# Kernel tuning notes

Measured on AMD Instinct MI355X. Metric: run time of the kernel, lower is better.

## Reference

```python
import jax, jax.numpy as jnp
import numpy as np


def setup_inputs() -> dict:
    key = jax.random.key(0)
    k1, k2, k3 = jax.random.split(key, 3)
    B, H, S, D = 2, 8, 4096, 64
    queries = jax.random.normal(k1, (B, H, S, D), dtype=jnp.float32)
    keys = jax.random.normal(k2, (B, H, S, D), dtype=jnp.float32)
    values = jax.random.normal(k3, (B, H, S, D), dtype=jnp.float32)
    mask = jnp.zeros((1, 1, S, S), dtype=jnp.float32)
    return {"queries": queries, "keys": keys, "values": values, "d_k": D, "mask": mask}


def reference(queries, keys, values, d_k, mask):
    # scores: [B, H, Sq, Sk]
    scale = 1.0 / jnp.sqrt(jnp.asarray(d_k, dtype=queries.dtype))
    scores = jnp.einsum("bhqd,bhkd->bhqk", queries, keys) * scale
    scores = scores + (-1e9) * mask  # additive mask, broadcasts over B, H
    weights = jax.nn.softmax(scores, axis=-1)
    return jnp.einsum("bhqk,bhkd->bhqd", weights, values)
```

## Files before the change

kernel.cpp:

```cpp
#include <hip/hip_runtime.h>

#define S_LEN 4096
#define DHEAD 64
#define BK    64
#define NT    (S_LEN / BK)
#define NBH   16
#define KPAD  72
#define BQ    128
#define TILE_HALFS (BK * DHEAD)
#define WS_KV_HALFS ((size_t)NBH * NT * TILE_HALFS)

typedef __fp16   pk16x2 __attribute__((ext_vector_type(2)));
typedef _Float16 half4v __attribute__((ext_vector_type(4)));
typedef _Float16 half8  __attribute__((ext_vector_type(8)));
typedef float    f32x4  __attribute__((ext_vector_type(4)));
typedef float    f32x16 __attribute__((ext_vector_type(16)));
typedef unsigned uint2v __attribute__((ext_vector_type(2)));

#define MFMA32(a, b, c) __builtin_amdgcn_mfma_f32_32x32x16_f16(a, b, c, 0, 0, 0)

__device__ __forceinline__ void gl_lds16(const _Float16* g, _Float16* l) {
    __builtin_amdgcn_global_load_lds(
        (const __attribute__((address_space(1))) unsigned int*)g,
        (__attribute__((address_space(3))) unsigned int*)l, 16, 0, 0);
}

__device__ __forceinline__ unsigned pk2u(float a, float b) {
    union { pk16x2 p; unsigned u; } x;
    x.p = __builtin_amdgcn_cvt_pkrtz(a, b);
    return x.u;
}

__device__ __forceinline__ uint2v pls(unsigned x, unsigned y) {
    return __builtin_amdgcn_permlane32_swap(x, y, false, false);
}
__device__ __forceinline__ float xmax32(float v) {
    uint2v r = pls(__float_as_uint(v), __float_as_uint(v));
    return fmaxf(__uint_as_float(r.x), __uint_as_float(r.y));
}
__device__ __forceinline__ float xadd32(float v) {
    uint2v r = pls(__float_as_uint(v), __float_as_uint(v));
    return __uint_as_float(r.x) + __uint_as_float(r.y);
}

__global__ void mask_flag_kernel(const float4* __restrict__ mask, int* __restrict__ flag) {
    const long stride = 2048L * 256;
    long i = (long)blockIdx.x * 256 + threadIdx.x;
    int nz = 0;
    #pragma unroll
    for (int it = 0; it < 8; ++it) {
        float4 a = mask[i + it * stride];
        nz |= (a.x != 0.f) | (a.y != 0.f) | (a.z != 0.f) | (a.w != 0.f);
    }
    if (__any(nz)) {
        if ((threadIdx.x & 63) == 0) atomicOr(flag, 1);
    }
}

__global__ void conv_kernel(const float* __restrict__ Kg, const float* __restrict__ Vg,
                            const float* __restrict__ mask,
                            _Float16* __restrict__ wsK, _Float16* __restrict__ wsV,
                            int* __restrict__ flag) {
    const int tid  = threadIdx.x;
    const int tile = blockIdx.x;
    __shared__ __align__(16) _Float16 T[64][64];

    if (blockIdx.y == 0) {
        const float* Ksrc = Kg + (long)tile * TILE_HALFS;
        _Float16*    dst  = wsK + (long)tile * TILE_HALFS;
        #pragma unroll
        for (int it = 0; it < 2; ++it) {
            int m = tid + it * 256;
            int r = m >> 3, c = m & 7;
            const float4* s4 = (const float4*)(Ksrc + r * DHEAD + ((c ^ (r & 7)) << 3));
            float4 a = s4[0], b = s4[1];
            union { pk16x2 p[4]; half8 h; } u;
            u.p[0] = __builtin_amdgcn_cvt_pkrtz(a.x, a.y);
            u.p[1] = __builtin_amdgcn_cvt_pkrtz(a.z, a.w);
            u.p[2] = __builtin_amdgcn_cvt_pkrtz(b.x, b.y);
            u.p[3] = __builtin_amdgcn_cvt_pkrtz(b.z, b.w);
            *(half8*)(dst + m * 8) = u.h;
        }
    } else if (blockIdx.y == 1) {
        const float* Vsrc = Vg + (long)tile * TILE_HALFS;
        const int r  = tid >> 2;
        const int d0 = (tid & 3) << 4;
        const float4* s4 = (const float4*)(Vsrc + r * DHEAD + d0);
        float vv[16];
        *(float4*)&vv[0]  = s4[0];
        *(float4*)&vv[4]  = s4[1];
        *(float4*)&vv[8]  = s4[2];
        *(float4*)&vv[12] = s4[3];
        #pragma unroll
        for (int j = 0; j < 16; j += 2) {
            pk16x2 p = __builtin_amdgcn_cvt_pkrtz(vv[j], vv[j + 1]);
            T[d0 + j][r]     = *((_Float16*)&p);
            T[d0 + j + 1][r] = *((_Float16*)&p + 1);
        }
        __syncthreads();
        _Float16* dst = wsV + (long)tile * TILE_HALFS;
        #pragma unroll
        for (int it = 0; it < 2; ++it) {
            int m = tid + it * 256;
            int d = m >> 3, c = m & 7;
            *(half8*)(dst + m * 8) = *(const half8*)&T[d][(c ^ (d & 7)) << 3];
        }
    } else {
        const float4* m4 = (const float4*)mask;
        const long stride = 1024L * 256;
        long i = (long)blockIdx.x * 256 + tid;
        int nz = 0;
        #pragma unroll
        for (int it = 0; it < 16; ++it) {
            float4 a = m4[i + it * stride];
            nz |= (a.x != 0.f) | (a.y != 0.f) | (a.z != 0.f) | (a.w != 0.f);
        }
        if (__any(nz)) {
            if ((tid & 63) == 0) atomicOr(flag, 1);
        }
    }
}

template <int SPLIT>
__global__ __launch_bounds__(256, 4) void attn32_kernel(
    const float* __restrict__ Q, const _Float16* __restrict__ KW,
    const _Float16* __restrict__ VW, const int* __restrict__ dkp,
    const float* __restrict__ mask, const int* __restrict__ maskflag,
    float* __restrict__ O1, float* __restrict__ O2, float* __restrict__ ML)
{
    const int fid = blockIdx.x;
    int bh, half, qt;
    if (SPLIT == 2) {
        const int L = (fid & 7) * 128 + (fid >> 3);
        bh = L >> 6; half = (L >> 5) & 1; qt = L & 31;
    } else {
        const int L = (fid & 7) * 64 + (fid >> 3);
        bh = L >> 5; half = 0; qt = L & 31;
    }
    const int HT  = NT / SPLIT;
    const int kt0 = half * HT;

    const int tid  = threadIdx.x;
    const int wave = tid >> 6;
    const int lane = tid & 63;
    const int l31  = lane & 31;
    const int h    = lane >> 5;
    const int cx   = lane & 7;
    const bool hib = (lane >= 32);

    const long base = (long)bh * S_LEN * DHEAD;
    const float* Qh = Q + base;
    const _Float16* gk = KW + (long)bh * (NT * TILE_HALFS);
    const _Float16* gv = VW + (long)bh * (NT * TILE_HALFS);

    const int q0 = qt * 128 + wave * 32;
    const float csq  = rsqrtf((float)dkp[0]) * 1.44269504088896f;
    const float mfac = -1e9f * 1.44269504088896f;
    const bool use_mask = (maskflag[0] != 0);

    __shared__ __align__(16) _Float16 KT[2][TILE_HALFS];
    __shared__ __align__(16) _Float16 VT[2][TILE_HALFS];

    half8 qf[4];
    #pragma unroll
    for (int ks = 0; ks < 4; ++ks) {
        const float4* src = (const float4*)(Qh + (long)(q0 + l31) * DHEAD + ks * 16 + h * 8);
        float4 a = src[0], b = src[1];
        union { unsigned u[4]; half8 h8; } u;
        u.u[0] = pk2u(a.x * csq, a.y * csq);
        u.u[1] = pk2u(a.z * csq, a.w * csq);
        u.u[2] = pk2u(b.x * csq, b.y * csq);
        u.u[3] = pk2u(b.z * csq, b.w * csq);
        qf[ks] = u.h8;
    }

    auto stage = [&](int kt, int bb) {
        const _Float16* k8 = gk + (long)kt * TILE_HALFS + tid * 8;
        const _Float16* v8 = gv + (long)kt * TILE_HALFS + tid * 8;
        gl_lds16(k8,        &KT[bb][tid * 8]);
        gl_lds16(k8 + 2048, &KT[bb][2048 + tid * 8]);
        gl_lds16(v8,        &VT[bb][tid * 8]);
        gl_lds16(v8 + 2048, &VT[bb][2048 + tid * 8]);
    };

    f32x16 o0 = {0.f,0.f,0.f,0.f,0.f,0.f,0.f,0.f,0.f,0.f,0.f,0.f,0.f,0.f,0.f,0.f};
    f32x16 o1 = o0;
    float m_i = -INFINITY;
    float l_i = 0.0f;

    stage(kt0, 0);
    __syncthreads();

    for (int lt = 0; lt < HT; ++lt) {
        const int kt = kt0 + lt;
        const int b  = lt & 1;
        if (lt + 1 < HT) stage(kt + 1, b ^ 1);

        f32x16 s0 = {0.f,0.f,0.f,0.f,0.f,0.f,0.f,0.f,0.f,0.f,0.f,0.f,0.f,0.f,0.f,0.f};
        f32x16 s1 = s0;
        __builtin_amdgcn_s_setprio(1);
        #pragma unroll
        for (int ks = 0; ks < 4; ++ks) {
            const int off = (((2 * ks + h) ^ cx) << 3);
            half8 a0 = *(const half8*)&KT[b][(l31 << 6) + off];
            half8 a1 = *(const half8*)&KT[b][2048 + (l31 << 6) + off];
            s0 = MFMA32(a0, qf[ks], s0);
            s1 = MFMA32(a1, qf[ks], s1);
        }
        __builtin_amdgcn_s_setprio(0);

        if (use_mask) {
            const float* mrow = mask + (long)(q0 + l31) * S_LEN + kt * BK;
            #pragma unroll
            for (int r = 0; r < 16; ++r) {
                const int k = (r & 3) + ((r >> 2) << 3) + (h << 2);
                s0[r] += mfac * mrow[k];
                s1[r] += mfac * mrow[32 + k];
            }
        }

        {
            float t[8];
            #pragma unroll
            for (int i = 0; i < 8; ++i)
                t[i] = fmaxf(fmaxf(s0[2*i], s0[2*i+1]), fmaxf(s1[2*i], s1[2*i+1]));
            float mx = fmaxf(fmaxf(fmaxf(t[0], t[1]), fmaxf(t[2], t[3])),
                             fmaxf(fmaxf(t[4], t[5]), fmaxf(t[6], t[7])));
            mx = xmax32(mx);
            const bool need = __any(mx > m_i);
            const float mnew = need ? fmaxf(m_i, mx) : m_i;
            float ra = 0.f, rb = 0.f;
            #pragma unroll
            for (int r = 0; r < 16; ++r) {
                float p0 = __builtin_amdgcn_exp2f(s0[r] - mnew);
                float p1 = __builtin_amdgcn_exp2f(s1[r] - mnew);
                s0[r] = p0; s1[r] = p1;
                ra += p0; rb += p1;
            }
            float rsum = xadd32(ra + rb);
            if (need) {
                const float alpha = __builtin_amdgcn_exp2f(m_i - mnew);
                #pragma unroll
                for (int r = 0; r < 16; ++r) {
                    const int qr = (r & 3) + ((r >> 2) << 3) + (h << 2);
                    float a_r = __shfl(alpha, qr, 64);
                    o0[r] *= a_r; o1[r] *= a_r;
                }
                l_i = alpha * l_i + rsum;
                m_i = mnew;
            } else {
                l_i += rsum;
            }
        }

        unsigned plo[16], phi[16];
        #pragma unroll
        for (int d = 0; d < 8; ++d) {
            uint2v r0 = pls(pk2u(s0[2*d], s0[2*d+1]), pk2u(s0[2*d], s0[2*d+1]));
            plo[d] = r0.x; phi[d] = r0.y;
            uint2v r1 = pls(pk2u(s1[2*d], s1[2*d+1]), pk2u(s1[2*d], s1[2*d+1]));
            plo[8 + d] = r1.x; phi[8 + d] = r1.y;
        }

        __builtin_amdgcn_s_setprio(1);
        #pragma unroll
        for (int s = 0; s < 4; ++s) {
            const int kb = s >> 1, tq = s & 1, bs = kb * 8 + 4 * tq;
            union { unsigned u[4]; half8 h8; } pa;
            pa.u[0] = hib ? plo[bs + 2] : plo[bs + 0];
            pa.u[1] = hib ? plo[bs + 3] : plo[bs + 1];
            pa.u[2] = hib ? phi[bs + 2] : phi[bs + 0];
            pa.u[3] = hib ? phi[bs + 3] : phi[bs + 1];
            const int off = (((2 * s + h) ^ cx) << 3);
            half8 v0 = *(const half8*)&VT[b][(l31 << 6) + off];
            half8 v1 = *(const half8*)&VT[b][2048 + (l31 << 6) + off];
            o0 = MFMA32(pa.h8, v0, o0);
            o1 = MFMA32(pa.h8, v1, o1);
        }
        __builtin_amdgcn_s_setprio(0);

        if (lt + 1 < HT) __syncthreads();
    }

    if (SPLIT == 2) {
        float* dst = ((half == 0) ? O1 : O2) + base;
        #pragma unroll
        for (int r = 0; r < 16; ++r) {
            const int qr = (r & 3) + ((r >> 2) << 3) + (h << 2);
            const long row = (long)(q0 + qr) * DHEAD;
            dst[row + l31]      = o0[r];
            dst[row + 32 + l31] = o1[r];
        }
        if (!hib) {
            float2* ml = (float2*)ML + (long)(half * NBH + bh) * S_LEN + q0 + l31;
            *ml = make_float2(m_i, l_i);
        }
    } else {
        float* dst = O1 + base;
        #pragma unroll
        for (int r = 0; r < 16; ++r) {
            const int qr = (r & 3) + ((r >> 2) << 3) + (h << 2);
            float lq = __shfl(l_i, qr, 64);
            float inv = __builtin_amdgcn_rcpf(lq);
            const long row = (long)(q0 + qr) * DHEAD;
            dst[row + l31]      = o0[r] * inv;
            dst[row + 32 + l31] = o1[r] * inv;
        }
    }
}

__global__ __launch_bounds__(256) void combine_kernel(
    float* __restrict__ O1, const float* __restrict__ O2,
    const float* __restrict__ ML)
{
    const long flat = (long)blockIdx.x * 256 + threadIdx.x;
    const int  dg = (int)(flat & 15);
    const long q  = (flat >> 4) & (S_LEN - 1);
    const int  bh = (int)(flat >> 16);
    const float2 ml1 = ((const float2*)ML)[(long)(0 * NBH + bh) * S_LEN + q];
    const float2 ml2 = ((const float2*)ML)[(long)(1 * NBH + bh) * S_LEN + q];
    const float m  = fmaxf(ml1.x, ml2.x);
    const float a1 = __builtin_amdgcn_exp2f(ml1.x - m);
    const float a2 = __builtin_amdgcn_exp2f(ml2.x - m);
    const float inv = __builtin_amdgcn_rcpf(ml1.y * a1 + ml2.y * a2);
    const long idx = ((long)bh * S_LEN + q) * DHEAD + dg * 4;
    float4 x1 = *(const float4*)&O1[idx];
    float4 x2 = *(const float4*)&O2[idx];
    float4 r;
    r.x = (x1.x * a1 + x2.x * a2) * inv;
    r.y = (x1.y * a1 + x2.y * a2) * inv;
    r.z = (x1.z * a1 + x2.z * a2) * inv;
    r.w = (x1.w * a1 + x2.w * a2) * inv;
    *(float4*)&O1[idx] = r;
}

__global__ __launch_bounds__(256, 2) void attn_kernel_fb(
    const float* __restrict__ Q, const float* __restrict__ K,
    const float* __restrict__ V, const int* __restrict__ dk,
    const float* __restrict__ mask, const int* __restrict__ maskflag,
    float* __restrict__ O)
{
    const int qt   = blockIdx.x;
    const int bh   = blockIdx.y;
    const int tid  = threadIdx.x;
    const int wave = tid >> 6;
    const int lane = tid & 63;
    const int l15  = lane & 15;
    const int quad = lane >> 4;

    const long base = (long)bh * S_LEN * DHEAD;
    const float* Qh = Q + base;
    const float* Kh = K + base;
    const float* Vh = V + base;
    float*       Oh = O + base;

    const int q0 = qt * BQ + wave * 32;
    const float csq  = rsqrtf((float)dk[0]) * 1.44269504088896f;
    const float mfac = -1e9f * 1.44269504088896f;
    const bool use_mask = (maskflag[0] != 0);

    __shared__ __align__(16) _Float16 Kt[2][BK][KPAD];
    __shared__ __align__(16) _Float16 Vt[2][DHEAD * KPAD];
    __shared__ __align__(16) _Float16 Pw[4][32][KPAD];

    half8 qf[2][2];
    #pragma unroll
    for (int f = 0; f < 2; ++f) {
        #pragma unroll
        for (int kc = 0; kc < 2; ++kc) {
            const float4* src = (const float4*)(Qh + (long)(q0 + f*16 + l15) * DHEAD + kc*32 + quad*8);
            float4 a = src[0], b = src[1];
            union { pk16x2 p[4]; half8 h; } u;
            u.p[0] = __builtin_amdgcn_cvt_pkrtz(a.x*csq, a.y*csq);
            u.p[1] = __builtin_amdgcn_cvt_pkrtz(a.z*csq, a.w*csq);
            u.p[2] = __builtin_amdgcn_cvt_pkrtz(b.x*csq, b.y*csq);
            u.p[3] = __builtin_amdgcn_cvt_pkrtz(b.z*csq, b.w*csq);
            qf[f][kc] = u.h;
        }
    }

    const int kr  = tid >> 2;
    const int ks  = tid & 3;
    const int vrp = tid >> 3;
    const int vdq = tid & 7;
    const float* Kb = Kh + (long)kr * DHEAD + ks * 16;
    const float* Vb = Vh + (long)(2 * vrp) * DHEAD + vdq * 8;
    const int vcol = (((vrp >> 2) ^ vdq) << 3) + ((2 * vrp) & 7);
    const int vd0  = vdq * 8;

    float4 kf[4], vf[4];
    auto load_tile = [&](int kt) {
        const float4* kp  = (const float4*)(Kb + (long)kt * BK * DHEAD);
        kf[0] = kp[0]; kf[1] = kp[1]; kf[2] = kp[2]; kf[3] = kp[3];
        const float4* vp0 = (const float4*)(Vb + (long)kt * BK * DHEAD);
        const float4* vp1 = (const float4*)(Vb + (long)kt * BK * DHEAD + DHEAD);
        vf[0] = vp0[0]; vf[1] = vp0[1]; vf[2] = vp1[0]; vf[3] = vp1[1];
    };
    auto store_tile = [&](int b) {
        union { pk16x2 p[4]; half8 h; } u0, u1;
        u0.p[0] = __builtin_amdgcn_cvt_pkrtz(kf[0].x, kf[0].y);
        u0.p[1] = __builtin_amdgcn_cvt_pkrtz(kf[0].z, kf[0].w);
        u0.p[2] = __builtin_amdgcn_cvt_pkrtz(kf[1].x, kf[1].y);
        u0.p[3] = __builtin_amdgcn_cvt_pkrtz(kf[1].z, kf[1].w);
        u1.p[0] = __builtin_amdgcn_cvt_pkrtz(kf[2].x, kf[2].y);
        u1.p[1] = __builtin_amdgcn_cvt_pkrtz(kf[2].z, kf[2].w);
        u1.p[2] = __builtin_amdgcn_cvt_pkrtz(kf[3].x, kf[3].y);
        u1.p[3] = __builtin_amdgcn_cvt_pkrtz(kf[3].z, kf[3].w);
        *(half8*)&Kt[b][kr][ks*16]     = u0.h;
        *(half8*)&Kt[b][kr][ks*16 + 8] = u1.h;
        _Float16* vt = &Vt[b][0];
        *(pk16x2*)&vt[(vd0+0)*KPAD + vcol] = __builtin_amdgcn_cvt_pkrtz(vf[0].x, vf[2].x);
        *(pk16x2*)&vt[(vd0+1)*KPAD + vcol] = __builtin_amdgcn_cvt_pkrtz(vf[0].y, vf[2].y);
        *(pk16x2*)&vt[(vd0+2)*KPAD + vcol] = __builtin_amdgcn_cvt_pkrtz(vf[0].z, vf[2].z);
        *(pk16x2*)&vt[(vd0+3)*KPAD + vcol] = __builtin_amdgcn_cvt_pkrtz(vf[0].w, vf[2].w);
        *(pk16x2*)&vt[(vd0+4)*KPAD + vcol] = __builtin_amdgcn_cvt_pkrtz(vf[1].x, vf[3].x);
        *(pk16x2*)&vt[(vd0+5)*KPAD + vcol] = __builtin_amdgcn_cvt_pkrtz(vf[1].y, vf[3].y);
        *(pk16x2*)&vt[(vd0+6)*KPAD + vcol] = __builtin_amdgcn_cvt_pkrtz(vf[1].z, vf[3].z);
        *(pk16x2*)&vt[(vd0+7)*KPAD + vcol] = __builtin_amdgcn_cvt_pkrtz(vf[1].w, vf[3].w);
    };

    f32x4 o[2][4];
    #pragma unroll
    for (int f = 0; f < 2; ++f)
        #pragma unroll
        for (int dt = 0; dt < 4; ++dt) o[f][dt] = (f32x4){0.f, 0.f, 0.f, 0.f};
    float m_i[2] = {-INFINITY, -INFINITY};
    float l_i[2] = {0.0f, 0.0f};

    load_tile(0);
    store_tile(0);
    __syncthreads();

    for (int kt = 0; kt < NT; ++kt) {
        const int b = kt & 1;
        if (kt + 1 < NT) load_tile(kt + 1);

        f32x4 st[2][4];
        #pragma unroll
        for (int f = 0; f < 2; ++f)
            #pragma unroll
            for (int nt = 0; nt < 4; ++nt) st[f][nt] = (f32x4){0.f,0.f,0.f,0.f};
        #pragma unroll
        for (int nt = 0; nt < 4; ++nt) {
            #pragma unroll
            for (int kc = 0; kc < 2; ++kc) {
                half8 af = *(const half8*)&Kt[b][nt*16 + l15][kc*32 + quad*8];
                st[0][nt] = __builtin_amdgcn_mfma_f32_16x16x32_f16(af, qf[0][kc], st[0][nt], 0, 0, 0);
                st[1][nt] = __builtin_amdgcn_mfma_f32_16x16x32_f16(af, qf[1][kc], st[1][nt], 0, 0, 0);
            }
        }

        if (use_mask) {
            #pragma unroll
            for (int f = 0; f < 2; ++f) {
                const long mrow = (long)(q0 + f*16 + l15) * S_LEN + kt*BK;
                #pragma unroll
                for (int nt = 0; nt < 4; ++nt)
                    #pragma unroll
                    for (int r = 0; r < 4; ++r)
                        st[f][nt][r] += mfac * mask[mrow + nt*16 + quad*4 + r];
            }
        }

        float alpha[2];
        #pragma unroll
        for (int f = 0; f < 2; ++f) {
            float mx = fmaxf(fmaxf(fmaxf(st[f][0][0], st[f][0][1]), fmaxf(st[f][0][2], st[f][0][3])),
                             fmaxf(fmaxf(st[f][1][0], st[f][1][1]), fmaxf(st[f][1][2], st[f][1][3])));
            float mx2 = fmaxf(fmaxf(fmaxf(st[f][2][0], st[f][2][1]), fmaxf(st[f][2][2], st[f][2][3])),
                              fmaxf(fmaxf(st[f][3][0], st[f][3][1]), fmaxf(st[f][3][2], st[f][3][3])));
            mx = fmaxf(mx, mx2);
            mx = fmaxf(mx, __shfl_xor(mx, 16, 64));
            mx = fmaxf(mx, __shfl_xor(mx, 32, 64));
            float mnew = fmaxf(m_i[f], mx);
            float rsum = 0.0f;
            #pragma unroll
            for (int nt = 0; nt < 4; ++nt) {
                #pragma unroll
                for (int r = 0; r < 4; ++r) {
                    float p = __builtin_amdgcn_exp2f(st[f][nt][r] - mnew);
                    st[f][nt][r] = p;
                    rsum += p;
                }
            }
            rsum += __shfl_xor(rsum, 16, 64);
            rsum += __shfl_xor(rsum, 32, 64);
            alpha[f] = __builtin_amdgcn_exp2f(m_i[f] - mnew);
            l_i[f] = alpha[f] * l_i[f] + rsum;
            m_i[f] = mnew;
        }

        #pragma unroll
        for (int f = 0; f < 2; ++f)
            #pragma unroll
            for (int r = 0; r < 4; ++r) {
                float a_r = __shfl(alpha[f], quad*4 + r, 64);
                #pragma unroll
                for (int dt = 0; dt < 4; ++dt) o[f][dt][r] *= a_r;
            }

        #pragma unroll
        for (int f = 0; f < 2; ++f)
            #pragma unroll
            for (int nt = 0; nt < 4; ++nt) {
                union { pk16x2 p[2]; half4v h; } up;
                up.p[0] = __builtin_amdgcn_cvt_pkrtz(st[f][nt][0], st[f][nt][1]);
                up.p[1] = __builtin_amdgcn_cvt_pkrtz(st[f][nt][2], st[f][nt][3]);
                *(half4v*)&Pw[wave][f*16 + l15][nt*16 + quad*4] = up.h;
            }

        #pragma unroll
        for (int kc2 = 0; kc2 < 2; ++kc2) {
            half8 pa0 = *(const half8*)&Pw[wave][l15][kc2*32 + quad*8];
            half8 pa1 = *(const half8*)&Pw[wave][16 + l15][kc2*32 + quad*8];
            #pragma unroll
            for (int dt = 0; dt < 4; ++dt) {
                const int row = dt*16 + l15;
                const int pb  = (4*kc2 + quad) ^ (row >> 3);
                half8 vb = *(const half8*)&Vt[b][row*KPAD + pb*8];
                o[0][dt] = __builtin_amdgcn_mfma_f32_16x16x32_f16(pa0, vb, o[0][dt], 0, 0, 0);
                o[1][dt] = __builtin_amdgcn_mfma_f32_16x16x32_f16(pa1, vb, o[1][dt], 0, 0, 0);
            }
        }

        if (kt + 1 < NT) {
            store_tile((kt + 1) & 1);
            __syncthreads();
        }
    }

    #pragma unroll
    for (int f = 0; f < 2; ++f) {
        #pragma unroll
        for (int r = 0; r < 4; ++r) {
            float lq = __shfl(l_i[f], quad*4 + r, 64);
            float linv = __builtin_amdgcn_rcpf(lq);
            const long row = (long)(q0 + f*16 + quad*4 + r) * DHEAD;
            #pragma unroll
            for (int dt = 0; dt < 4; ++dt)
                Oh[row + dt*16 + l15] = o[f][dt][r] * linv;
        }
    }
}

extern "C" void kernel_launch(void* const* d_in, const int* in_sizes, int n_in,
                              void* d_out, int out_size, void* d_ws, size_t ws_size,
                              hipStream_t stream) {
    const float* Q    = (const float*)d_in[0];
    const float* K    = (const float*)d_in[1];
    const float* V    = (const float*)d_in[2];
    const int*   dk   = (const int*)d_in[3];
    const float* mask = (const float*)d_in[4];
    float* out = (float*)d_out;
    int* flag = (int*)d_ws;

    (void)hipMemsetAsync(flag, 0, sizeof(int), stream);

    const size_t KV_BYTES = 2 * WS_KV_HALFS * sizeof(_Float16);
    const size_t O2_BYTES = (size_t)NBH * S_LEN * DHEAD * sizeof(float);
    const size_t ML_BYTES = 2ull * NBH * S_LEN * 2 * sizeof(float);
    const size_t NEED_BASE  = 256 + KV_BYTES;
    const size_t NEED_SPLIT = NEED_BASE + O2_BYTES + ML_BYTES;

    if (ws_size >= NEED_BASE) {
        _Float16* wsK = (_Float16*)((char*)d_ws + 256);
        _Float16* wsV = wsK + WS_KV_HALFS;
        conv_kernel<<<dim3(NBH * NT, 3), 256, 0, stream>>>(K, V, mask, wsK, wsV, flag);
        if (ws_size >= NEED_SPLIT) {
            float* O2 = (float*)((char*)d_ws + 256 + KV_BYTES);
            float* ML = (float*)((char*)d_ws + 256 + KV_BYTES + O2_BYTES);
            attn32_kernel<2><<<1024, 256, 0, stream>>>(Q, wsK, wsV, dk, mask, flag, out, O2, ML);
            combine_kernel<<<4096, 256, 0, stream>>>(out, O2, ML);
        } else {
            attn32_kernel<1><<<512, 256, 0, stream>>>(Q, wsK, wsV, dk, mask, flag, out, nullptr, nullptr);
        }
    } else {
        mask_flag_kernel<<<2048, 256, 0, stream>>>((const float4*)mask, flag);
        dim3 grid(S_LEN / BQ, NBH);
        attn_kernel_fb<<<grid, 256, 0, stream>>>(Q, K, V, dk, mask, flag, out);
    }
}
```

Measured before the change: 270.6 us.

## Fuse split-KV combine into attention kernel via last-block atomic counter

The separate combine kernel is removed. Each block pair that shares a query tile now bumps an atomic counter, and whichever block finishes second merges the two partial outputs in place. The row-sum l is now accumulated with an extra MFMA against a ones vector instead of a VALU reduction. Rescaling is skipped unless the running max grows by more than 8, a lazy-rescale threshold. The P permutation is also simplified. These changes aim to cut a kernel launch and a full extra pass over O, plus VALU work, at the cost of one more MFMA per step and a tail where only some blocks do the combine.

```diff
diff --git a/kernel.cpp b/kernel.cpp
--- a/kernel.cpp
+++ b/kernel.cpp
@@ -121,24 +121,19 @@
     }
 }
 
-template <int SPLIT>
-__global__ __launch_bounds__(256, 4) void attn32_kernel(
+__global__ __launch_bounds__(256, 4) void attn32c_kernel(
     const float* __restrict__ Q, const _Float16* __restrict__ KW,
     const _Float16* __restrict__ VW, const int* __restrict__ dkp,
-    const float* __restrict__ mask, const int* __restrict__ maskflag,
+    const float* __restrict__ mask, int* __restrict__ ctrl,
     float* __restrict__ O1, float* __restrict__ O2, float* __restrict__ ML)
 {
-    const int fid = blockIdx.x;
-    int bh, half, qt;
-    if (SPLIT == 2) {
-        const int L = (fid & 7) * 128 + (fid >> 3);
-        bh = L >> 6; half = (L >> 5) & 1; qt = L & 31;
-    } else {
-        const int L = (fid & 7) * 64 + (fid >> 3);
-        bh = L >> 5; half = 0; qt = L & 31;
-    }
-    const int HT  = NT / SPLIT;
-    const int kt0 = half * HT;
+    const int bid = blockIdx.x;
+    const int L   = (bid & 7) * 128 + (bid >> 3);
+    const int bh  = L >> 6;
+    const int hf  = (L >> 5) & 1;
+    const int qt  = L & 31;
+    const int HT  = NT / 2;
+    const int kt0 = hf * HT;
 
     const int tid  = threadIdx.x;
     const int wave = tid >> 6;
@@ -146,20 +141,20 @@
     const int l31  = lane & 31;
     const int h    = lane >> 5;
     const int cx   = lane & 7;
-    const bool hib = (lane >= 32);
-
-    const long base = (long)bh * S_LEN * DHEAD;
-    const float* Qh = Q + base;
+
+    const long gbase = (long)bh * S_LEN * DHEAD;
+    const float* Qh = Q + gbase;
     const _Float16* gk = KW + (long)bh * (NT * TILE_HALFS);
     const _Float16* gv = VW + (long)bh * (NT * TILE_HALFS);
 
     const int q0 = qt * 128 + wave * 32;
     const float csq  = rsqrtf((float)dkp[0]) * 1.44269504088896f;
     const float mfac = -1e9f * 1.44269504088896f;
-    const bool use_mask = (maskflag[0] != 0);
+    const bool use_mask = (ctrl[0] != 0);
 
     __shared__ __align__(16) _Float16 KT[2][TILE_HALFS];
     __shared__ __align__(16) _Float16 VT[2][TILE_HALFS];
+    __shared__ int s_last;
 
     half8 qf[4];
     #pragma unroll
@@ -174,6 +169,10 @@
         qf[ks] = u.h8;
     }
 
+    half8 vones;
+    #pragma unroll
+    for (int j = 0; j < 8; ++j) vones[j] = (_Float16)1.0f;
+
     auto stage = [&](int kt, int bb) {
         const _Float16* k8 = gk + (long)kt * TILE_HALFS + tid * 8;
         const _Float16* v8 = gv + (long)kt * TILE_HALFS + tid * 8;
@@ -185,8 +184,8 @@
 
     f32x16 o0 = {0.f,0.f,0.f,0.f,0.f,0.f,0.f,0.f,0.f,0.f,0.f,0.f,0.f,0.f,0.f,0.f};
     f32x16 o1 = o0;
+    f32x16 ol = o0;
     float m_i = -INFINITY;
-    float l_i = 0.0f;
 
     stage(kt0, 0);
     __syncthreads();
@@ -211,6 +210,204 @@
 
         if (use_mask) {
             const float* mrow = mask + (long)(q0 + l31) * S_LEN + kt * BK;
+            #pragma unroll
+            for (int r = 0; r < 16; ++r) {
+                const int k = (r & 3) + ((r >> 2) << 3) + (h << 2);
+                s0[r] += mfac * mrow[k];
+                s1[r] += mfac * mrow[32 + k];
+            }
+        }
+
+        {
+            float t[8];
+            #pragma unroll
+            for (int i = 0; i < 8; ++i)
+                t[i] = fmaxf(fmaxf(s0[2*i], s0[2*i+1]), fmaxf(s1[2*i], s1[2*i+1]));
+            float mx = fmaxf(fmaxf(fmaxf(t[0], t[1]), fmaxf(t[2], t[3])),
+                             fmaxf(fmaxf(t[4], t[5]), fmaxf(t[6], t[7])));
+            mx = xmax32(mx);
+            const bool need = __any(mx > m_i + 8.0f);
+            const float mnew = need ? fmaxf(m_i, mx) : m_i;
+            #pragma unroll
+            for (int r = 0; r < 16; ++r) {
+                s0[r] = __builtin_amdgcn_exp2f(s0[r] - mnew);
+                s1[r] = __builtin_amdgcn_exp2f(s1[r] - mnew);
+            }
+            if (need) {
+                const float alpha = __builtin_amdgcn_exp2f(m_i - mnew);
+                #pragma unroll
+                for (int r = 0; r < 16; ++r) {
+                    const int qr = (r & 3) + ((r >> 2) << 3) + (h << 2);
+                    float a_r = __shfl(alpha, qr, 64);
+                    o0[r] *= a_r; o1[r] *= a_r; ol[r] *= a_r;
+                }
+                m_i = mnew;
+            }
+        }
+
+        unsigned w[16];
+        #pragma unroll
+        for (int d = 0; d < 8; ++d) {
+            w[d]     = pk2u(s0[2*d], s0[2*d+1]);
+            w[8 + d] = pk2u(s1[2*d], s1[2*d+1]);
+        }
+
+        __builtin_amdgcn_s_setprio(1);
+        #pragma unroll
+        for (int si = 0; si < 4; ++si) {
+            const int bs = (si >> 1) * 8 + (si & 1) * 4;
+            uint2v r0 = pls(w[bs + 0], w[bs + 2]);
+            uint2v r1 = pls(w[bs + 1], w[bs + 3]);
+            union { unsigned u[4]; half8 h8; } pa;
+            pa.u[0] = r0.x; pa.u[1] = r1.x; pa.u[2] = r0.y; pa.u[3] = r1.y;
+            const int off = (((2 * si + h) ^ cx) << 3);
+            half8 v0 = *(const half8*)&VT[b][(l31 << 6) + off];
+            half8 v1 = *(const half8*)&VT[b][2048 + (l31 << 6) + off];
+            o0 = MFMA32(pa.h8, v0, o0);
+            o1 = MFMA32(pa.h8, v1, o1);
+            ol = MFMA32(pa.h8, vones, ol);
+        }
+        __builtin_amdgcn_s_setprio(0);
+
+        if (lt + 1 < HT) __syncthreads();
+    }
+
+    float* dst = ((hf == 0) ? O1 : O2) + gbase;
+    #pragma unroll
+    for (int r = 0; r < 16; ++r) {
+        const int qr = (r & 3) + ((r >> 2) << 3) + (h << 2);
+        const long row = (long)(q0 + qr) * DHEAD;
+        dst[row + l31]      = o0[r];
+        dst[row + 32 + l31] = o1[r];
+    }
+    {
+        const int rr = l31 & 15;
+        float lv = ol[0];
+        #pragma unroll
+        for (int r = 1; r < 16; ++r) lv = (rr == r) ? ol[r] : lv;
+        const int qre = (rr & 3) + ((rr >> 2) << 3) + (h << 2);
+        const float mv = __shfl(m_i, qre, 64);
+        if (l31 < 16) {
+            float2* ml = (float2*)ML + (long)(hf * NBH + bh) * S_LEN + q0 + qre;
+            *ml = make_float2(mv, lv);
+        }
+    }
+
+    __syncthreads();
+    if (tid == 0) {
+        __threadfence();
+        int old = atomicAdd(ctrl + 64 + (bh * 32 + qt), 1);
+        if (old == 1) __threadfence();
+        s_last = old;
+    }
+    __syncthreads();
+
+    if (s_last == 1) {
+        const int q  = qt * 128 + (tid >> 1);
+        const int dc = (tid & 1) * 32;
+        const float2 ml1 = ((const float2*)ML)[(long)(0 * NBH + bh) * S_LEN + q];
+        const float2 ml2 = ((const float2*)ML)[(long)(NBH + bh) * S_LEN + q];
+        const float m   = fmaxf(ml1.x, ml2.x);
+        const float a1  = __builtin_amdgcn_exp2f(ml1.x - m);
+        const float a2  = __builtin_amdgcn_exp2f(ml2.x - m);
+        const float inv = __builtin_amdgcn_rcpf(ml1.y * a1 + ml2.y * a2);
+        float*       p1 = O1 + gbase + (long)q * DHEAD + dc;
+        const float* p2 = O2 + gbase + (long)q * DHEAD + dc;
+        #pragma unroll
+        for (int j = 0; j < 8; ++j) {
+            float4 x1 = *(const float4*)&p1[j * 4];
+            float4 x2 = *(const float4*)&p2[j * 4];
+            float4 r4;
+            r4.x = (x1.x * a1 + x2.x * a2) * inv;
+            r4.y = (x1.y * a1 + x2.y * a2) * inv;
+            r4.z = (x1.z * a1 + x2.z * a2) * inv;
+            r4.w = (x1.w * a1 + x2.w * a2) * inv;
+            *(float4*)&p1[j * 4] = r4;
+        }
+    }
+}
+
+__global__ __launch_bounds__(256, 4) void attn32_s1_kernel(
+    const float* __restrict__ Q, const _Float16* __restrict__ KW,
+    const _Float16* __restrict__ VW, const int* __restrict__ dkp,
+    const float* __restrict__ mask, const int* __restrict__ maskflag,
+    float* __restrict__ O1)
+{
+    const int fid = blockIdx.x;
+    const int L = (fid & 7) * 64 + (fid >> 3);
+    const int bh = L >> 5;
+    const int qt = L & 31;
+
+    const int tid  = threadIdx.x;
+    const int wave = tid >> 6;
+    const int lane = tid & 63;
+    const int l31  = lane & 31;
+    const int h    = lane >> 5;
+    const int cx   = lane & 7;
+    const bool hib = (lane >= 32);
+
+    const long base = (long)bh * S_LEN * DHEAD;
+    const float* Qh = Q + base;
+    const _Float16* gk = KW + (long)bh * (NT * TILE_HALFS);
+    const _Float16* gv = VW + (long)bh * (NT * TILE_HALFS);
+
+    const int q0 = qt * 128 + wave * 32;
+    const float csq  = rsqrtf((float)dkp[0]) * 1.44269504088896f;
+    const float mfac = -1e9f * 1.44269504088896f;
+    const bool use_mask = (maskflag[0] != 0);
+
+    __shared__ __align__(16) _Float16 KT[2][TILE_HALFS];
+    __shared__ __align__(16) _Float16 VT[2][TILE_HALFS];
+
+    half8 qf[4];
+    #pragma unroll
+    for (int ks = 0; ks < 4; ++ks) {
+        const float4* src = (const float4*)(Qh + (long)(q0 + l31) * DHEAD + ks * 16 + h * 8);
+        float4 a = src[0], b = src[1];
+        union { unsigned u[4]; half8 h8; } u;
+        u.u[0] = pk2u(a.x * csq, a.y * csq);
+        u.u[1] = pk2u(a.z * csq, a.w * csq);
+        u.u[2] = pk2u(b.x * csq, b.y * csq);
+        u.u[3] = pk2u(b.z * csq, b.w * csq);
+        qf[ks] = u.h8;
+    }
+
+    auto stage = [&](int kt, int bb) {
+        const _Float16* k8 = gk + (long)kt * TILE_HALFS + tid * 8;
+        const _Float16* v8 = gv + (long)kt * TILE_HALFS + tid * 8;
+        gl_lds16(k8,        &KT[bb][tid * 8]);
+        gl_lds16(k8 + 2048, &KT[bb][2048 + tid * 8]);
+        gl_lds16(v8,        &VT[bb][tid * 8]);
+        gl_lds16(v8 + 2048, &VT[bb][2048 + tid * 8]);
+    };
+
+    f32x16 o0 = {0.f,0.f,0.f,0.f,0.f,0.f,0.f,0.f,0.f,0.f,0.f,0.f,0.f,0.f,0.f,0.f};
+    f32x16 o1 = o0;
+    float m_i = -INFINITY;
+    float l_i = 0.0f;
+
+    stage(0, 0);
+    __syncthreads();
+
+    for (int lt = 0; lt < NT; ++lt) {
+        const int b = lt & 1;
+        if (lt + 1 < NT) stage(lt + 1, b ^ 1);
+
+        f32x16 s0 = {0.f,0.f,0.f,0.f,0.f,0.f,0.f,0.f,0.f,0.f,0.f,0.f,0.f,0.f,0.f,0.f};
+        f32x16 s1 = s0;
+        __builtin_amdgcn_s_setprio(1);
+        #pragma unroll
+        for (int ks = 0; ks < 4; ++ks) {
+            const int off = (((2 * ks + h) ^ cx) << 3);
+            half8 a0 = *(const half8*)&KT[b][(l31 << 6) + off];
+            half8 a1 = *(const half8*)&KT[b][2048 + (l31 << 6) + off];
+            s0 = MFMA32(a0, qf[ks], s0);
+            s1 = MFMA32(a1, qf[ks], s1);
+        }
+        __builtin_amdgcn_s_setprio(0);
+
+        if (use_mask) {
+            const float* mrow = mask + (long)(q0 + l31) * S_LEN + lt * BK;
             #pragma unroll
             for (int r = 0; r < 16; ++r) {
                 const int k = (r & 3) + ((r >> 2) << 3) + (h << 2);
@@ -265,7 +462,7 @@
         __builtin_amdgcn_s_setprio(1);
         #pragma unroll
         for (int s = 0; s < 4; ++s) {
-            const int kb = s >> 1, tq = s & 1, bs = kb * 8 + 4 * tq;
+            const int bs = (s >> 1) * 8 + (s & 1) * 4;
             union { unsigned u[4]; half8 h8; } pa;
             pa.u[0] = hib ? plo[bs + 2] : plo[bs + 0];
             pa.u[1] = hib ? plo[bs + 3] : plo[bs + 1];
@@ -279,59 +476,19 @@
         }
         __builtin_amdgcn_s_setprio(0);
 
-        if (lt + 1 < HT) __syncthreads();
-    }
-
-    if (SPLIT == 2) {
-        float* dst = ((half == 0) ? O1 : O2) + base;
-        #pragma unroll
-        for (int r = 0; r < 16; ++r) {
-            const int qr = (r & 3) + ((r >> 2) << 3) + (h << 2);
-            const long row = (long)(q0 + qr) * DHEAD;
-            dst[row + l31]      = o0[r];
-            dst[row + 32 + l31] = o1[r];
-        }
-        if (!hib) {
-            float2* ml = (float2*)ML + (long)(half * NBH + bh) * S_LEN + q0 + l31;
-            *ml = make_float2(m_i, l_i);
-        }
-    } else {
-        float* dst = O1 + base;
-        #pragma unroll
-        for (int r = 0; r < 16; ++r) {
-            const int qr = (r & 3) + ((r >> 2) << 3) + (h << 2);
-            float lq = __shfl(l_i, qr, 64);
-            float inv = __builtin_amdgcn_rcpf(lq);
-            const long row = (long)(q0 + qr) * DHEAD;
-            dst[row + l31]      = o0[r] * inv;
-            dst[row + 32 + l31] = o1[r] * inv;
-        }
-    }
-}
-
-__global__ __launch_bounds__(256) void combine_kernel(
-    float* __restrict__ O1, const float* __restrict__ O2,
-    const float* __restrict__ ML)
-{
-    const long flat = (long)blockIdx.x * 256 + threadIdx.x;
-    const int  dg = (int)(flat & 15);
-    const long q  = (flat >> 4) & (S_LEN - 1);
-    const int  bh = (int)(flat >> 16);
-    const float2 ml1 = ((const float2*)ML)[(long)(0 * NBH + bh) * S_LEN + q];
-    const float2 ml2 = ((const float2*)ML)[(long)(1 * NBH + bh) * S_LEN + q];
-    const float m  = fmaxf(ml1.x, ml2.x);
-    const float a1 = __builtin_amdgcn_exp2f(ml1.x - m);
-    const float a2 = __builtin_amdgcn_exp2f(ml2.x - m);
-    const float inv = __builtin_amdgcn_rcpf(ml1.y * a1 + ml2.y * a2);
-    const long idx = ((long)bh * S_LEN + q) * DHEAD + dg * 4;
-    float4 x1 = *(const float4*)&O1[idx];
-    float4 x2 = *(const float4*)&O2[idx];
-    float4 r;
-    r.x = (x1.x * a1 + x2.x * a2) * inv;
-    r.y = (x1.y * a1 + x2.y * a2) * inv;
-    r.z = (x1.z * a1 + x2.z * a2) * inv;
-    r.w = (x1.w * a1 + x2.w * a2) * inv;
-    *(float4*)&O1[idx] = r;
+        if (lt + 1 < NT) __syncthreads();
+    }
+
+    float* dst = O1 + base;
+    #pragma unroll
+    for (int r = 0; r < 16; ++r) {
+        const int qr = (r & 3) + ((r >> 2) << 3) + (h << 2);
+        float lq = __shfl(l_i, qr, 64);
+        float inv = __builtin_amdgcn_rcpf(lq);
+        const long row = (long)(q0 + qr) * DHEAD;
+        dst[row + l31]      = o0[r] * inv;
+        dst[row + 32 + l31] = o1[r] * inv;
+    }
 }
 
 __global__ __launch_bounds__(256, 2) void attn_kernel_fb(
@@ -552,31 +709,31 @@
     const int*   dk   = (const int*)d_in[3];
     const float* mask = (const float*)d_in[4];
     float* out = (float*)d_out;
-    int* flag = (int*)d_ws;
-
-    (void)hipMemsetAsync(flag, 0, sizeof(int), stream);
-
+    int* ctrl = (int*)d_ws;
+
+    (void)hipMemsetAsync(ctrl, 0, 4096, stream);
+
+    const size_t CTRL     = 4096;
     const size_t KV_BYTES = 2 * WS_KV_HALFS * sizeof(_Float16);
     const size_t O2_BYTES = (size_t)NBH * S_LEN * DHEAD * sizeof(float);
     const size_t ML_BYTES = 2ull * NBH * S_LEN * 2 * sizeof(float);
-    const size_t NEED_BASE  = 256 + KV_BYTES;
-    const size_t NEED_SPLIT = NEED_BASE + O2_BYTES + ML_BYTES;
+    const size_t NEED_BASE = CTRL + KV_BYTES;
+    const size_t NEED_FULL = NEED_BASE + O2_BYTES + ML_BYTES;
 
     if (ws_size >= NEED_BASE) {
-        _Float16* wsK = (_Float16*)((char*)d_ws + 256);
+        _Float16* wsK = (_Float16*)((char*)d_ws + CTRL);
         _Float16* wsV = wsK + WS_KV_HALFS;
-        conv_kernel<<<dim3(NBH * NT, 3), 256, 0, stream>>>(K, V, mask, wsK, wsV, flag);
-        if (ws_size >= NEED_SPLIT) {
-            float* O2 = (float*)((char*)d_ws + 256 + KV_BYTES);
-            float* ML = (float*)((char*)d_ws + 256 + KV_BYTES + O2_BYTES);
-            attn32_kernel<2><<<1024, 256, 0, stream>>>(Q, wsK, wsV, dk, mask, flag, out, O2, ML);
-            combine_kernel<<<4096, 256, 0, stream>>>(out, O2, ML);
+        conv_kernel<<<dim3(NBH * NT, 3), 256, 0, stream>>>(K, V, mask, wsK, wsV, ctrl);
+        if (ws_size >= NEED_FULL) {
+            float* O2 = (float*)((char*)d_ws + CTRL + KV_BYTES);
+            float* ML = (float*)((char*)d_ws + CTRL + KV_BYTES + O2_BYTES);
+            attn32c_kernel<<<1024, 256, 0, stream>>>(Q, wsK, wsV, dk, mask, ctrl, out, O2, ML);
         } else {
-            attn32_kernel<1><<<512, 256, 0, stream>>>(Q, wsK, wsV, dk, mask, flag, out, nullptr, nullptr);
+            attn32_s1_kernel<<<512, 256, 0, stream>>>(Q, wsK, wsV, dk, mask, ctrl, out);
         }
     } else {
-        mask_flag_kernel<<<2048, 256, 0, stream>>>((const float4*)mask, flag);
+        mask_flag_kernel<<<2048, 256, 0, stream>>>((const float4*)mask, ctrl);
         dim3 grid(S_LEN / BQ, NBH);
-        attn_kernel_fb<<<grid, 256, 0, stream>>>(Q, K, V, dk, mask, flag, out);
-    }
-}
+        attn_kernel_fb<<<grid, 256, 0, stream>>>(Q, K, V, dk, mask, ctrl, out);
+    }
+}
```

Result: slower. 323.7 us (+19.6%).

## Fuse split-KV halves into one 512-thread block with in-LDS combine

Applied to the files above, without the earlier changes.

Replaces the two-pass split-KV attention (1024 blocks of 256 threads plus a separate combine kernel through global O2/ML buffers) with one 512-thread block per query tile. Each 256-thread half processes half the key tiles and the two partial results are merged through shared memory at the end. The change also computes the row sums with an extra MFMA against a ones vector instead of shuffle reductions, and skips the max rescale unless the new max exceeds the old one by more than 8 in the exp2 domain. It removes the extra kernel launch and the global round-trip of partial outputs. In exchange it doubles LDS per block, which may reduce occupancy, and the lazy rescale relies on fp16 probabilities staying in range.

```diff
diff --git a/kernel.cpp b/kernel.cpp
--- a/kernel.cpp
+++ b/kernel.cpp
@@ -37,10 +37,6 @@
 __device__ __forceinline__ float xmax32(float v) {
     uint2v r = pls(__float_as_uint(v), __float_as_uint(v));
     return fmaxf(__uint_as_float(r.x), __uint_as_float(r.y));
-}
-__device__ __forceinline__ float xadd32(float v) {
-    uint2v r = pls(__float_as_uint(v), __float_as_uint(v));
-    return __uint_as_float(r.x) + __uint_as_float(r.y);
 }
 
 __global__ void mask_flag_kernel(const float4* __restrict__ mask, int* __restrict__ flag) {
@@ -121,45 +117,41 @@
     }
 }
 
-template <int SPLIT>
-__global__ __launch_bounds__(256, 4) void attn32_kernel(
+__global__ __launch_bounds__(512, 4) void attn32x_kernel(
     const float* __restrict__ Q, const _Float16* __restrict__ KW,
     const _Float16* __restrict__ VW, const int* __restrict__ dkp,
     const float* __restrict__ mask, const int* __restrict__ maskflag,
-    float* __restrict__ O1, float* __restrict__ O2, float* __restrict__ ML)
+    float* __restrict__ O)
 {
-    const int fid = blockIdx.x;
-    int bh, half, qt;
-    if (SPLIT == 2) {
-        const int L = (fid & 7) * 128 + (fid >> 3);
-        bh = L >> 6; half = (L >> 5) & 1; qt = L & 31;
-    } else {
-        const int L = (fid & 7) * 64 + (fid >> 3);
-        bh = L >> 5; half = 0; qt = L & 31;
-    }
-    const int HT  = NT / SPLIT;
-    const int kt0 = half * HT;
+    const int bid = blockIdx.x;
+    const int L   = (bid & 7) * 64 + (bid >> 3);
+    const int bh  = L >> 5;
+    const int qt  = L & 31;
 
     const int tid  = threadIdx.x;
-    const int wave = tid >> 6;
+    const int hf   = tid >> 8;
+    const int t    = tid & 255;
+    const int w    = (tid >> 6) & 3;
     const int lane = tid & 63;
     const int l31  = lane & 31;
     const int h    = lane >> 5;
     const int cx   = lane & 7;
-    const bool hib = (lane >= 32);
-
-    const long base = (long)bh * S_LEN * DHEAD;
-    const float* Qh = Q + base;
+
+    const int HT  = NT / 2;
+    const int kt0 = hf * HT;
+
+    const long gbase = (long)bh * S_LEN * DHEAD;
+    const float* Qh = Q + gbase;
     const _Float16* gk = KW + (long)bh * (NT * TILE_HALFS);
     const _Float16* gv = VW + (long)bh * (NT * TILE_HALFS);
 
-    const int q0 = qt * 128 + wave * 32;
+    const int q0 = qt * 128 + w * 32;
     const float csq  = rsqrtf((float)dkp[0]) * 1.44269504088896f;
     const float mfac = -1e9f * 1.44269504088896f;
     const bool use_mask = (maskflag[0] != 0);
 
-    __shared__ __align__(16) _Float16 KT[2][TILE_HALFS];
-    __shared__ __align__(16) _Float16 VT[2][TILE_HALFS];
+    __shared__ __align__(16) _Float16 KT[2][2][TILE_HALFS];
+    __shared__ __align__(16) _Float16 VT[2][2][TILE_HALFS];
 
     half8 qf[4];
     #pragma unroll
@@ -174,19 +166,23 @@
         qf[ks] = u.h8;
     }
 
+    half8 vones;
+    #pragma unroll
+    for (int j = 0; j < 8; ++j) vones[j] = (_Float16)1.0f;
+
     auto stage = [&](int kt, int bb) {
-        const _Float16* k8 = gk + (long)kt * TILE_HALFS + tid * 8;
-        const _Float16* v8 = gv + (long)kt * TILE_HALFS + tid * 8;
-        gl_lds16(k8,        &KT[bb][tid * 8]);
-        gl_lds16(k8 + 2048, &KT[bb][2048 + tid * 8]);
-        gl_lds16(v8,        &VT[bb][tid * 8]);
-        gl_lds16(v8 + 2048, &VT[bb][2048 + tid * 8]);
+        const _Float16* k8 = gk + (long)kt * TILE_HALFS + t * 8;
+        const _Float16* v8 = gv + (long)kt * TILE_HALFS + t * 8;
+        gl_lds16(k8,        &KT[hf][bb][t * 8]);
+        gl_lds16(k8 + 2048, &KT[hf][bb][2048 + t * 8]);
+        gl_lds16(v8,        &VT[hf][bb][t * 8]);
+        gl_lds16(v8 + 2048, &VT[hf][bb][2048 + t * 8]);
     };
 
     f32x16 o0 = {0.f,0.f,0.f,0.f,0.f,0.f,0.f,0.f,0.f,0.f,0.f,0.f,0.f,0.f,0.f,0.f};
     f32x16 o1 = o0;
+    f32x16 ol = o0;
     float m_i = -INFINITY;
-    float l_i = 0.0f;
 
     stage(kt0, 0);
     __syncthreads();
@@ -202,8 +198,8 @@
         #pragma unroll
         for (int ks = 0; ks < 4; ++ks) {
             const int off = (((2 * ks + h) ^ cx) << 3);
-            half8 a0 = *(const half8*)&KT[b][(l31 << 6) + off];
-            half8 a1 = *(const half8*)&KT[b][2048 + (l31 << 6) + off];
+            half8 a0 = *(const half8*)&KT[hf][b][(l31 << 6) + off];
+            half8 a1 = *(const half8*)&KT[hf][b][2048 + (l31 << 6) + off];
             s0 = MFMA32(a0, qf[ks], s0);
             s1 = MFMA32(a1, qf[ks], s1);
         }
@@ -220,118 +216,101 @@
         }
 
         {
-            float t[8];
+            float tt[8];
             #pragma unroll
             for (int i = 0; i < 8; ++i)
-                t[i] = fmaxf(fmaxf(s0[2*i], s0[2*i+1]), fmaxf(s1[2*i], s1[2*i+1]));
-            float mx = fmaxf(fmaxf(fmaxf(t[0], t[1]), fmaxf(t[2], t[3])),
-                             fmaxf(fmaxf(t[4], t[5]), fmaxf(t[6], t[7])));
+                tt[i] = fmaxf(fmaxf(s0[2*i], s0[2*i+1]), fmaxf(s1[2*i], s1[2*i+1]));
+            float mx = fmaxf(fmaxf(fmaxf(tt[0], tt[1]), fmaxf(tt[2], tt[3])),
+                             fmaxf(fmaxf(tt[4], tt[5]), fmaxf(tt[6], tt[7])));
             mx = xmax32(mx);
-            const bool need = __any(mx > m_i);
+            const bool need = __any(mx > m_i + 8.0f);
             const float mnew = need ? fmaxf(m_i, mx) : m_i;
-            float ra = 0.f, rb = 0.f;
             #pragma unroll
             for (int r = 0; r < 16; ++r) {
-                float p0 = __builtin_amdgcn_exp2f(s0[r] - mnew);
-                float p1 = __builtin_amdgcn_exp2f(s1[r] - mnew);
-                s0[r] = p0; s1[r] = p1;
-                ra += p0; rb += p1;
-            }
-            float rsum = xadd32(ra + rb);
+                s0[r] = __builtin_amdgcn_exp2f(s0[r] - mnew);
+                s1[r] = __builtin_amdgcn_exp2f(s1[r] - mnew);
+            }
             if (need) {
                 const float alpha = __builtin_amdgcn_exp2f(m_i - mnew);
                 #pragma unroll
                 for (int r = 0; r < 16; ++r) {
                     const int qr = (r & 3) + ((r >> 2) << 3) + (h << 2);
                     float a_r = __shfl(alpha, qr, 64);
-                    o0[r] *= a_r; o1[r] *= a_r;
+                    o0[r] *= a_r; o1[r] *= a_r; ol[r] *= a_r;
                 }
-                l_i = alpha * l_i + rsum;
                 m_i = mnew;
-            } else {
-                l_i += rsum;
-            }
-        }
-
-        unsigned plo[16], phi[16];
+            }
+        }
+
+        unsigned wp[16];
         #pragma unroll
         for (int d = 0; d < 8; ++d) {
-            uint2v r0 = pls(pk2u(s0[2*d], s0[2*d+1]), pk2u(s0[2*d], s0[2*d+1]));
-            plo[d] = r0.x; phi[d] = r0.y;
-            uint2v r1 = pls(pk2u(s1[2*d], s1[2*d+1]), pk2u(s1[2*d], s1[2*d+1]));
-            plo[8 + d] = r1.x; phi[8 + d] = r1.y;
+            wp[d]     = pk2u(s0[2*d], s0[2*d+1]);
+            wp[8 + d] = pk2u(s1[2*d], s1[2*d+1]);
         }
 
         __builtin_amdgcn_s_setprio(1);
         #pragma unroll
-        for (int s = 0; s < 4; ++s) {
-            const int kb = s >> 1, tq = s & 1, bs = kb * 8 + 4 * tq;
+        for (int si = 0; si < 4; ++si) {
+            const int bs = (si >> 1) * 8 + (si & 1) * 4;
+            uint2v r0 = pls(wp[bs + 0], wp[bs + 2]);
+            uint2v r1 = pls(wp[bs + 1], wp[bs + 3]);
             union { unsigned u[4]; half8 h8; } pa;
-            pa.u[0] = hib ? plo[bs + 2] : plo[bs + 0];
-            pa.u[1] = hib ? plo[bs + 3] : plo[bs + 1];
-            pa.u[2] = hib ? phi[bs + 2] : phi[bs + 0];
-            pa.u[3] = hib ? phi[bs + 3] : phi[bs + 1];
-            const int off = (((2 * s + h) ^ cx) << 3);
-            half8 v0 = *(const half8*)&VT[b][(l31 << 6) + off];
-            half8 v1 = *(const half8*)&VT[b][2048 + (l31 << 6) + off];
+            pa.u[0] = r0.x; pa.u[1] = r1.x; pa.u[2] = r0.y; pa.u[3] = r1.y;
+            const int off = (((2 * si + h) ^ cx) << 3);
+            half8 v0 = *(const half8*)&VT[hf][b][(l31 << 6) + off];
+            half8 v1 = *(const half8*)&VT[hf][b][2048 + (l31 << 6) + off];
             o0 = MFMA32(pa.h8, v0, o0);
             o1 = MFMA32(pa.h8, v1, o1);
+            ol = MFMA32(pa.h8, vones, ol);
         }
         __builtin_amdgcn_s_setprio(0);
 
         if (lt + 1 < HT) __syncthreads();
     }
 
-    if (SPLIT == 2) {
-        float* dst = ((half == 0) ? O1 : O2) + base;
+    const int  rr  = (l31 & 3) + ((l31 >> 3) << 2);
+    const bool own = (((l31 >> 2) & 1) == h);
+    float lv = ol[0];
+    #pragma unroll
+    for (int r = 1; r < 16; ++r) lv = (rr == r) ? ol[r] : lv;
+
+    float*  comb = (float*)&KT[0][0][0];
+    float2* mlA  = (float2*)&VT[0][0][0];
+    float2* mlB  = mlA + 128;
+
+    __syncthreads();
+    if (hf == 1) {
         #pragma unroll
         for (int r = 0; r < 16; ++r) {
             const int qr = (r & 3) + ((r >> 2) << 3) + (h << 2);
-            const long row = (long)(q0 + qr) * DHEAD;
-            dst[row + l31]      = o0[r];
-            dst[row + 32 + l31] = o1[r];
-        }
-        if (!hib) {
-            float2* ml = (float2*)ML + (long)(half * NBH + bh) * S_LEN + q0 + l31;
-            *ml = make_float2(m_i, l_i);
-        }
+            comb[w * 2048 + qr * 64 + l31]      = o0[r];
+            comb[w * 2048 + qr * 64 + 32 + l31] = o1[r];
+        }
+        if (own) mlB[w * 32 + l31] = make_float2(m_i, lv);
     } else {
-        float* dst = O1 + base;
+        if (own) mlA[w * 32 + l31] = make_float2(m_i, lv);
+    }
+    __syncthreads();
+
+    if (hf == 0) {
+        float* dst = O + gbase;
         #pragma unroll
         for (int r = 0; r < 16; ++r) {
             const int qr = (r & 3) + ((r >> 2) << 3) + (h << 2);
-            float lq = __shfl(l_i, qr, 64);
-            float inv = __builtin_amdgcn_rcpf(lq);
+            const float2 ml1 = mlA[w * 32 + qr];
+            const float2 ml2 = mlB[w * 32 + qr];
+            const float m   = fmaxf(ml1.x, ml2.x);
+            const float a1  = __builtin_amdgcn_exp2f(ml1.x - m);
+            const float a2  = __builtin_amdgcn_exp2f(ml2.x - m);
+            const float inv = __builtin_amdgcn_rcpf(ml1.y * a1 + ml2.y * a2);
+            const float p0  = comb[w * 2048 + qr * 64 + l31];
+            const float p1  = comb[w * 2048 + qr * 64 + 32 + l31];
             const long row = (long)(q0 + qr) * DHEAD;
-            dst[row + l31]      = o0[r] * inv;
-            dst[row + 32 + l31] = o1[r] * inv;
-        }
-    }
-}
-
-__global__ __launch_bounds__(256) void combine_kernel(
-    float* __restrict__ O1, const float* __restrict__ O2,
-    const float* __restrict__ ML)
-{
-    const long flat = (long)blockIdx.x * 256 + threadIdx.x;
-    const int  dg = (int)(flat & 15);
-    const long q  = (flat >> 4) & (S_LEN - 1);
-    const int  bh = (int)(flat >> 16);
-    const float2 ml1 = ((const float2*)ML)[(long)(0 * NBH + bh) * S_LEN + q];
-    const float2 ml2 = ((const float2*)ML)[(long)(1 * NBH + bh) * S_LEN + q];
-    const float m  = fmaxf(ml1.x, ml2.x);
-    const float a1 = __builtin_amdgcn_exp2f(ml1.x - m);
-    const float a2 = __builtin_amdgcn_exp2f(ml2.x - m);
-    const float inv = __builtin_amdgcn_rcpf(ml1.y * a1 + ml2.y * a2);
-    const long idx = ((long)bh * S_LEN + q) * DHEAD + dg * 4;
-    float4 x1 = *(const float4*)&O1[idx];
-    float4 x2 = *(const float4*)&O2[idx];
-    float4 r;
-    r.x = (x1.x * a1 + x2.x * a2) * inv;
-    r.y = (x1.y * a1 + x2.y * a2) * inv;
-    r.z = (x1.z * a1 + x2.z * a2) * inv;
-    r.w = (x1.w * a1 + x2.w * a2) * inv;
-    *(float4*)&O1[idx] = r;
+            dst[row + l31]      = (o0[r] * a1 + p0 * a2) * inv;
+            dst[row + 32 + l31] = (o1[r] * a1 + p1 * a2) * inv;
+        }
+    }
 }
 
 __global__ __launch_bounds__(256, 2) void attn_kernel_fb(
@@ -552,31 +531,22 @@
     const int*   dk   = (const int*)d_in[3];
     const float* mask = (const float*)d_in[4];
     float* out = (float*)d_out;
-    int* flag = (int*)d_ws;
-
-    (void)hipMemsetAsync(flag, 0, sizeof(int), stream);
-
-    const size_t KV_BYTES = 2 * WS_KV_HALFS * sizeof(_Float16);
-    const size_t O2_BYTES = (size_t)NBH * S_LEN * DHEAD * sizeof(float);
-    const size_t ML_BYTES = 2ull * NBH * S_LEN * 2 * sizeof(float);
-    const size_t NEED_BASE  = 256 + KV_BYTES;
-    const size_t NEED_SPLIT = NEED_BASE + O2_BYTES + ML_BYTES;
+    int* ctrl = (int*)d_ws;
+
+    (void)hipMemsetAsync(ctrl, 0, 256, stream);
+
+    const size_t CTRL      = 256;
+    const size_t KV_BYTES  = 2 * WS_KV_HALFS * sizeof(_Float16);
+    const size_t NEED_BASE = CTRL + KV_BYTES;
 
     if (ws_size >= NEED_BASE) {
-        _Float16* wsK = (_Float16*)((char*)d_ws + 256);
+        _Float16* wsK = (_Float16*)((char*)d_ws + CTRL);
         _Float16* wsV = wsK + WS_KV_HALFS;
-        conv_kernel<<<dim3(NBH * NT, 3), 256, 0, stream>>>(K, V, mask, wsK, wsV, flag);
-        if (ws_size >= NEED_SPLIT) {
-            float* O2 = (float*)((char*)d_ws + 256 + KV_BYTES);
-            float* ML = (float*)((char*)d_ws + 256 + KV_BYTES + O2_BYTES);
-            attn32_kernel<2><<<1024, 256, 0, stream>>>(Q, wsK, wsV, dk, mask, flag, out, O2, ML);
-            combine_kernel<<<4096, 256, 0, stream>>>(out, O2, ML);
-        } else {
-            attn32_kernel<1><<<512, 256, 0, stream>>>(Q, wsK, wsV, dk, mask, flag, out, nullptr, nullptr);
-        }
+        conv_kernel<<<dim3(NBH * NT, 3), 256, 0, stream>>>(K, V, mask, wsK, wsV, ctrl);
+        attn32x_kernel<<<512, 512, 0, stream>>>(Q, wsK, wsV, dk, mask, ctrl, out);
     } else {
-        mask_flag_kernel<<<2048, 256, 0, stream>>>((const float4*)mask, flag);
+        mask_flag_kernel<<<2048, 256, 0, stream>>>((const float4*)mask, ctrl);
         dim3 grid(S_LEN / BQ, NBH);
-        attn_kernel_fb<<<grid, 256, 0, stream>>>(Q, K, V, dk, mask, flag, out);
-    }
-}
+        attn_kernel_fb<<<grid, 256, 0, stream>>>(Q, K, V, dk, mask, ctrl, out);
+    }
+}
```

New measurement: 274.6 us. About the same (+1.5%).
